# Kernel tuning notes

Hardware: AMD Instinct MI355X
Metric: run time of the kernel (lower is better)

Reference implementation:

```python
import jax, jax.numpy as jnp
import numpy as np

B, T, C = 4, 2048, 2048
N_HEAD = 16
HEAD_DIM = C // N_HEAD
ROPE_BASE = 10000.0


def setup_inputs() -> dict:
    key = jax.random.key(0)
    k1, k2, k3 = jax.random.split(key, 3)
    x = jax.random.normal(k1, (B, T, C), dtype=jnp.float32)
    Wqkv = jax.random.normal(k2, (C, 3 * C), dtype=jnp.float32) * 0.02
    bqkv = jnp.zeros((3 * C,), dtype=jnp.float32)
    Wproj = jax.random.normal(k3, (C, C), dtype=jnp.float32) * 0.02
    bproj = jnp.zeros((C,), dtype=jnp.float32)
    return {"x": x, "Wqkv": Wqkv, "bqkv": bqkv, "Wproj": Wproj, "bproj": bproj}


def _rope_cos_sin(seq_len, head_dim, dtype):
    inv_freq = 1.0 / (ROPE_BASE ** (jnp.arange(0, head_dim, 2, dtype=jnp.float32) / head_dim))
    t = jnp.arange(seq_len, dtype=jnp.float32)
    freqs = jnp.einsum("i,j->ij", t, inv_freq)          # [T, D/2]
    emb = jnp.concatenate([freqs, freqs], axis=-1)       # [T, D]
    return jnp.cos(emb).astype(dtype), jnp.sin(emb).astype(dtype)


def _rotate_half(x):
    half = x.shape[-1] // 2
    x1, x2 = x[..., :half], x[..., half:]
    return jnp.concatenate([-x2, x1], axis=-1)


def reference(x, Wqkv, bqkv, Wproj, bproj):
    b, t, c = x.shape
    qkv = x @ Wqkv + bqkv                                # [B, T, 3C]
    q, k, v = jnp.split(qkv, 3, axis=-1)
    # [B, T, C] -> [B, H, T, D]
    def to_heads(u):
        return u.reshape(b, t, N_HEAD, HEAD_DIM).transpose(0, 2, 1, 3)
    q, k, v = to_heads(q), to_heads(k), to_heads(v)
    cos, sin = _rope_cos_sin(t, HEAD_DIM, x.dtype)       # [T, D]
    cos = cos[None, None]                                # [1, 1, T, D]
    sin = sin[None, None]
    q = q * cos + _rotate_half(q) * sin
    k = k * cos + _rotate_half(k) * sin
    scale = 1.0 / np.sqrt(HEAD_DIM).astype(np.float32)
    scores = jnp.einsum("bhqd,bhkd->bhqk", q, k) * scale  # [B, H, T, T]
    causal = jnp.tril(jnp.ones((t, t), dtype=bool))
    scores = jnp.where(causal[None, None], scores, jnp.finfo(scores.dtype).min)
    att = jax.nn.softmax(scores, axis=-1)
    y = jnp.einsum("bhqk,bhkd->bhqd", att, v)             # [B, H, T, D]
    y = y.transpose(0, 2, 1, 3).reshape(b, t, c)
    return y @ Wproj + bproj
```

## Files before the change

kernel.cpp:

```cpp
#include <hip/hip_runtime.h>
#include <hip/hip_bf16.h>
#include <stdint.h>
#include <math.h>

#define NB 4
#define NT 2048
#define NC 2048
#define NH 16
#define HD 128
#define BT (NB*NT)

typedef __attribute__((ext_vector_type(8))) short s16x8;
typedef __attribute__((ext_vector_type(4))) short s16x4;
typedef __attribute__((ext_vector_type(4))) float f32x4;

typedef __attribute__((address_space(1))) void as1_void;
typedef __attribute__((address_space(3))) void as3_void;

static __device__ __forceinline__ unsigned short f2bf(float f) {
  union { float f; uint32_t u; } v; v.f = f;
  return (unsigned short)((v.u + 0x7fffu + ((v.u >> 16) & 1u)) >> 16);
}
static __device__ __forceinline__ float bf2f(unsigned short u) {
  union { uint32_t u; float f; } v; v.u = ((uint32_t)u) << 16;
  return v.f;
}
static __device__ __forceinline__ void async16(unsigned short* lds, const unsigned short* g) {
  __builtin_amdgcn_global_load_lds((as1_void*)g, (as3_void*)lds, 16, 0, 0);
}
static __device__ __forceinline__ uint32_t lds_off(void* p) {
  return (uint32_t)(size_t)(as3_void*)p;
}

__global__ void k_convert_bf16(const float* __restrict__ in, unsigned short* __restrict__ out, int n8) {
  int i = blockIdx.x * blockDim.x + threadIdx.x;
  if (i >= n8) return;
  const float4* p = (const float4*)in + (size_t)i * 2;
  float4 a = p[0], b = p[1];
  union { unsigned short s[8]; uint4 u; } o;
  o.s[0] = f2bf(a.x); o.s[1] = f2bf(a.y); o.s[2] = f2bf(a.z); o.s[3] = f2bf(a.w);
  o.s[4] = f2bf(b.x); o.s[5] = f2bf(b.y); o.s[6] = f2bf(b.z); o.s[7] = f2bf(b.w);
  ((uint4*)out)[i] = o.u;
}

__global__ void k_transpose_bf16(const float* __restrict__ W, unsigned short* __restrict__ WT, int K, int N) {
  __shared__ unsigned short tile[64][65];
  const int k0 = blockIdx.y * 64, n0 = blockIdx.x * 64;
  const int t = threadIdx.x;
  const int jj = t & 63, base_i = t >> 6;
  #pragma unroll
  for (int p = 0; p < 16; ++p) {
    int i = p * 4 + base_i;
    tile[i][jj] = f2bf(W[(size_t)(k0 + i) * N + n0 + jj]);
  }
  __syncthreads();
  #pragma unroll
  for (int p = 0; p < 16; ++p) {
    int j = p * 4 + base_i;
    WT[(size_t)(n0 + j) * K + k0 + jj] = tile[jj][j];
  }
}

__global__ void k_rope(unsigned short* __restrict__ Q, unsigned short* __restrict__ Kb) {
  int idx = blockIdx.x * 256 + threadIdx.x;
  int d = idx & 63;
  int tpos = (idx >> 6) & (NT - 1);
  int bh = idx >> 17;
  size_t o = ((size_t)bh * NT + tpos) * HD + d;
  float invf = exp2f(-(float)d * 0.2076205059304602f);
  float ang = (float)tpos * invf;
  float s, c;
  sincosf(ang, &s, &c);
  float q1 = bf2f(Q[o]),  q2 = bf2f(Q[o + 64]);
  float k1 = bf2f(Kb[o]), k2 = bf2f(Kb[o + 64]);
  const float qs = 0.08838834764831845f * 1.4426950408889634f;
  Q[o]       = f2bf((q1 * c - q2 * s) * qs);
  Q[o + 64]  = f2bf((q2 * c + q1 * s) * qs);
  Kb[o]      = f2bf(k1 * c - k2 * s);
  Kb[o + 64] = f2bf(k2 * c + k1 * s);
}

template<int MODE>
__global__ __launch_bounds__(256, 2)
void k_gemm_bt2(const unsigned short* __restrict__ A,
                const unsigned short* __restrict__ Bt,
                const float* __restrict__ bias,
                float* __restrict__ OutF,
                unsigned short* __restrict__ Qd,
                unsigned short* __restrict__ Kd,
                unsigned short* __restrict__ Vd,
                int M, int N, int K)
{
  __shared__ __align__(16) unsigned short Al[256 * 64];
  __shared__ __align__(16) unsigned short Bl[128 * 64];
  const int t = threadIdx.x;
  const int l = t & 63;
  const int wv = t >> 6;
  const int wm = wv >> 1, wn = wv & 1;
  const int bm = blockIdx.y * 256, bn = blockIdx.x * 128;
  const int lr = l & 15, lg = l >> 4;

  f32x4 acc[8][4];
  #pragma unroll
  for (int i = 0; i < 8; ++i)
    #pragma unroll
    for (int j = 0; j < 4; ++j)
      acc[i][j] = f32x4{0.f, 0.f, 0.f, 0.f};

  for (int k0 = 0; k0 < K; k0 += 64) {
    #pragma unroll
    for (int i = 0; i < 8; ++i) {
      const int Cc = i * 256 + t;
      const int row = Cc >> 3;
      const int kc = (Cc & 7) ^ (row & 7);
      async16(&Al[(i * 256 + (t & 192)) * 8], &A[(size_t)(bm + row) * K + k0 + kc * 8]);
    }
    #pragma unroll
    for (int i = 0; i < 4; ++i) {
      const int Cc = i * 256 + t;
      const int row = Cc >> 3;
      const int kc = (Cc & 7) ^ (row & 7);
      async16(&Bl[(i * 256 + (t & 192)) * 8], &Bt[(size_t)(bn + row) * K + k0 + kc * 8]);
    }
    __syncthreads();
    #pragma unroll
    for (int kk = 0; kk < 2; ++kk) {
      s16x8 af[8], bfr[4];
      #pragma unroll
      for (int mi = 0; mi < 8; ++mi) {
        const int row = wm * 128 + mi * 16 + lr;
        const int ch = (kk * 4 + lg) ^ (row & 7);
        af[mi] = *(const s16x8*)&Al[row * 64 + ch * 8];
      }
      #pragma unroll
      for (int ni = 0; ni < 4; ++ni) {
        const int row = wn * 64 + ni * 16 + lr;
        const int ch = (kk * 4 + lg) ^ (row & 7);
        bfr[ni] = *(const s16x8*)&Bl[row * 64 + ch * 8];
      }
      __builtin_amdgcn_s_setprio(1);
      #pragma unroll
      for (int mi = 0; mi < 8; ++mi)
        #pragma unroll
        for (int ni = 0; ni < 4; ++ni)
          acc[mi][ni] = __builtin_amdgcn_mfma_f32_16x16x32_bf16(af[mi], bfr[ni], acc[mi][ni], 0, 0, 0);
      __builtin_amdgcn_s_setprio(0);
    }
    __syncthreads();
  }

  #pragma unroll
  for (int mi = 0; mi < 8; ++mi) {
    #pragma unroll
    for (int ni = 0; ni < 4; ++ni) {
      const int col = bn + wn * 64 + ni * 16 + lr;
      const float bv = bias[col];
      #pragma unroll
      for (int r = 0; r < 4; ++r) {
        const int row = bm + wm * 128 + mi * 16 + lg * 4 + r;
        const float v = acc[mi][ni][r] + bv;
        if (MODE == 1) {
          OutF[(size_t)row * N + col] = v;
        } else {
          const int which = col >> 11;
          const int cc = col & 2047;
          const int h = cc >> 7, d = cc & 127;
          const int b = row >> 11, tp = row & 2047;
          unsigned short* dst = (which == 0) ? Qd : (which == 1 ? Kd : Vd);
          dst[(((size_t)(b * NH + h)) * NT + tp) * HD + d] = f2bf(v);
        }
      }
    }
  }
}

__global__ __launch_bounds__(256, 2)
void k_attn(const unsigned short* __restrict__ Q,
            const unsigned short* __restrict__ Kg,
            const unsigned short* __restrict__ Vg,
            unsigned short* __restrict__ Yatt)
{
  __shared__ __align__(16) unsigned short Kl[64 * 128];
  __shared__ __align__(16) unsigned short Vl[64 * 128];
  const int bh = blockIdx.x;
  const int pair = blockIdx.y;
  const int b = bh >> 4, h = bh & 15;
  const int t = threadIdx.x, l = t & 63, wv = t >> 6;
  const int lr = l & 15, lg = l >> 4;
  const size_t hoff = (size_t)bh * NT * HD;
  const unsigned short* Qh = Q + hoff;
  const unsigned short* Kh = Kg + hoff;
  const unsigned short* Vh = Vg + hoff;
  const uint32_t vbase = lds_off(Vl);

  #pragma unroll 1
  for (int rep = 0; rep < 2; ++rep) {
    const int qb = rep ? (31 - pair) : pair;
    const int q0w = qb * 64 + wv * 16;
    const int qrow = q0w + lr;

    s16x8 qf[4];
    #pragma unroll
    for (int m = 0; m < 4; ++m)
      qf[m] = *(const s16x8*)(Qh + (size_t)qrow * HD + m * 32 + lg * 8);

    f32x4 yt[8];
    #pragma unroll
    for (int n = 0; n < 8; ++n) yt[n] = f32x4{0.f, 0.f, 0.f, 0.f};
    float mrun = -1e30f, lrun = 0.f;

    const int nkv = qb + 1;
    for (int kv = 0; kv < nkv; ++kv) {
      const int kv0 = kv * 64;
      #pragma unroll
      for (int i = 0; i < 4; ++i) {
        const int Cc = i * 256 + t;
        {
          const int krow = Cc >> 4;
          const int kc = (Cc & 15) ^ (krow & 7);
          async16(&Kl[(i * 256 + (t & 192)) * 8], &Kh[(size_t)(kv0 + krow) * HD + kc * 8]);
        }
        {
          const int S = Cc >> 3, c8 = Cc & 7;
          const int kq = S >> 3, dq = S & 7;
          const int vk = kq * 4 + (c8 >> 1), vd = dq * 16 + (c8 & 1) * 8;
          async16(&Vl[(i * 256 + (t & 192)) * 8], &Vh[(size_t)(kv0 + vk) * HD + vd]);
        }
      }
      __syncthreads();

      f32x4 st[4];
      __builtin_amdgcn_s_setprio(1);
      #pragma unroll
      for (int kt = 0; kt < 4; ++kt) {
        f32x4 a = f32x4{0.f, 0.f, 0.f, 0.f};
        const int krow = kt * 16 + lr;
        #pragma unroll
        for (int m = 0; m < 4; ++m) {
          const int ch = (m * 4 + lg) ^ (krow & 7);
          s16x8 kf = *(const s16x8*)&Kl[krow * 128 + ch * 8];
          a = __builtin_amdgcn_mfma_f32_16x16x32_bf16(kf, qf[m], a, 0, 0, 0);
        }
        st[kt] = a;
      }
      __builtin_amdgcn_s_setprio(0);

      if (kv0 + 63 > q0w) {
        #pragma unroll
        for (int kt = 0; kt < 4; ++kt)
          #pragma unroll
          for (int r = 0; r < 4; ++r) {
            const int key = kv0 + kt * 16 + lg * 4 + r;
            if (key > qrow) st[kt][r] = -3.0e38f;
          }
      }

      float tm = -3.0e38f;
      #pragma unroll
      for (int kt = 0; kt < 4; ++kt)
        #pragma unroll
        for (int r = 0; r < 4; ++r) tm = fmaxf(tm, st[kt][r]);
      tm = fmaxf(tm, __shfl_xor(tm, 16));
      tm = fmaxf(tm, __shfl_xor(tm, 32));
      const float mnew = fmaxf(mrun, tm);
      const float fsc = exp2f(mrun - mnew);
      mrun = mnew;
      lrun *= fsc;
      #pragma unroll
      for (int n = 0; n < 8; ++n)
        #pragma unroll
        for (int r = 0; r < 4; ++r) yt[n][r] *= fsc;

      unsigned short pb[16];
      float psum = 0.f;
      #pragma unroll
      for (int kt = 0; kt < 4; ++kt)
        #pragma unroll
        for (int r = 0; r < 4; ++r) {
          const float p = exp2f(st[kt][r] - mnew);
          psum += p;
          pb[kt * 4 + r] = f2bf(p);
        }
      lrun += psum;

      s16x8 pf[2];
      #pragma unroll
      for (int gk = 0; gk < 2; ++gk)
        #pragma unroll
        for (int j = 0; j < 8; ++j)
          pf[gk][j] = (short)pb[(gk * 2 + (j >> 2)) * 4 + (j & 3)];

      #pragma unroll
      for (int gk = 0; gk < 2; ++gk) {
        s16x4 va[8], vb2[8];
        #pragma unroll
        for (int n = 0; n < 8; ++n) {
          const uint32_t a0 = vbase + ((uint32_t)((gk * 8 + lg) * 8 + n)) * 128 + (uint32_t)lr * 8;
          asm volatile("ds_read_b64_tr_b16 %0, %1" : "=v"(va[n])  : "v"(a0));
          asm volatile("ds_read_b64_tr_b16 %0, %1" : "=v"(vb2[n]) : "v"(a0 + 4096));
        }
        asm volatile("s_waitcnt lgkmcnt(0)" ::: "memory");
        __builtin_amdgcn_sched_barrier(0);
        __builtin_amdgcn_s_setprio(1);
        #pragma unroll
        for (int n = 0; n < 8; ++n) {
          s16x8 vf;
          vf[0] = va[n][0];  vf[1] = va[n][1];  vf[2] = va[n][2];  vf[3] = va[n][3];
          vf[4] = vb2[n][0]; vf[5] = vb2[n][1]; vf[6] = vb2[n][2]; vf[7] = vb2[n][3];
          yt[n] = __builtin_amdgcn_mfma_f32_16x16x32_bf16(vf, pf[gk], yt[n], 0, 0, 0);
        }
        __builtin_amdgcn_s_setprio(0);
      }
      __syncthreads();
    }

    lrun += __shfl_xor(lrun, 16);
    lrun += __shfl_xor(lrun, 32);
    const float inv = 1.f / lrun;
    unsigned short* yrow = Yatt + (size_t)(b * NT + q0w + lr) * NC + h * HD;
    #pragma unroll
    for (int n = 0; n < 8; ++n)
      #pragma unroll
      for (int r = 0; r < 4; ++r)
        yrow[n * 16 + lg * 4 + r] = f2bf(yt[n][r] * inv);
  }
}

extern "C" void kernel_launch(void* const* d_in, const int* in_sizes, int n_in,
                              void* d_out, int out_size, void* d_ws, size_t ws_size,
                              hipStream_t stream) {
  (void)in_sizes; (void)n_in; (void)out_size; (void)ws_size;
  const float* x     = (const float*)d_in[0];
  const float* Wqkv  = (const float*)d_in[1];
  const float* bqkv  = (const float*)d_in[2];
  const float* Wproj = (const float*)d_in[3];
  const float* bproj = (const float*)d_in[4];
  float* out = (float*)d_out;
  char* ws = (char*)d_ws;

  unsigned short* xb     = (unsigned short*)(ws);
  unsigned short* WqkvT  = (unsigned short*)(ws + 33554432);
  unsigned short* WprojT = (unsigned short*)(ws + 58720256);
  unsigned short* Qb     = (unsigned short*)(ws + 67108864);
  unsigned short* Kb     = (unsigned short*)(ws + 100663296);
  unsigned short* Vb     = (unsigned short*)(ws + 134217728);
  unsigned short* att    = xb;

  k_convert_bf16<<<dim3(8192), dim3(256), 0, stream>>>(x, xb, BT * NC / 8);
  k_transpose_bf16<<<dim3(96, 32), dim3(256), 0, stream>>>(Wqkv, WqkvT, NC, 3 * NC);
  k_transpose_bf16<<<dim3(32, 32), dim3(256), 0, stream>>>(Wproj, WprojT, NC, NC);
  k_gemm_bt2<0><<<dim3(48, 32), dim3(256), 0, stream>>>(xb, WqkvT, bqkv, nullptr, Qb, Kb, Vb, BT, 3 * NC, NC);
  k_rope<<<dim3(32768), dim3(256), 0, stream>>>(Qb, Kb);
  k_attn<<<dim3(64, 16), dim3(256), 0, stream>>>(Qb, Kb, Vb, att);
  k_gemm_bt2<1><<<dim3(16, 32), dim3(256), 0, stream>>>(att, WprojT, bproj, out, nullptr, nullptr, nullptr, BT, NC, NC);
}
```

Before: 446.6 us.

## Double-buffer K/V tiles in attention to overlap loads with compute

The attention kernel now keeps two LDS buffers for K and V and issues async loads for the next KV tile before computing the current one, with a single barrier per iteration. The goal is to hide global-to-LDS load latency behind the MFMA and softmax work. Two smaller changes ride along: the GEMM launch bound occupancy hint goes from 2 to 3 blocks, and the RoPE kernel uses the fast __sincosf intrinsic. The extra buffers double the attention kernel's LDS use, which can reduce occupancy. __sincosf is also less accurate for large angles.

Result: slower. 1.188 ms (+166.1%).

```diff
diff --git a/kernel.cpp b/kernel.cpp
--- a/kernel.cpp
+++ b/kernel.cpp
@@ -70,7 +70,7 @@
   float invf = exp2f(-(float)d * 0.2076205059304602f);
   float ang = (float)tpos * invf;
   float s, c;
-  sincosf(ang, &s, &c);
+  __sincosf(ang, &s, &c);
   float q1 = bf2f(Q[o]),  q2 = bf2f(Q[o + 64]);
   float k1 = bf2f(Kb[o]), k2 = bf2f(Kb[o + 64]);
   const float qs = 0.08838834764831845f * 1.4426950408889634f;
@@ -81,7 +81,7 @@
 }
 
 template<int MODE>
-__global__ __launch_bounds__(256, 2)
+__global__ __launch_bounds__(256, 3)
 void k_gemm_bt2(const unsigned short* __restrict__ A,
                 const unsigned short* __restrict__ Bt,
                 const float* __restrict__ bias,
@@ -180,8 +180,8 @@
             const unsigned short* __restrict__ Vg,
             unsigned short* __restrict__ Yatt)
 {
-  __shared__ __align__(16) unsigned short Kl[64 * 128];
-  __shared__ __align__(16) unsigned short Vl[64 * 128];
+  __shared__ __align__(16) unsigned short Kl[2][64 * 128];
+  __shared__ __align__(16) unsigned short Vl[2][64 * 128];
   const int bh = blockIdx.x;
   const int pair = blockIdx.y;
   const int b = bh >> 4, h = bh & 15;
@@ -191,7 +191,25 @@
   const unsigned short* Qh = Q + hoff;
   const unsigned short* Kh = Kg + hoff;
   const unsigned short* Vh = Vg + hoff;
-  const uint32_t vbase = lds_off(Vl);
+  const uint32_t vbase0 = lds_off(&Vl[0][0]);
+
+  auto stageKV = [&](int buf, int kv0) {
+    #pragma unroll
+    for (int i = 0; i < 4; ++i) {
+      const int Cc = i * 256 + t;
+      {
+        const int krow = Cc >> 4;
+        const int kc = (Cc & 15) ^ (krow & 7);
+        async16(&Kl[buf][(i * 256 + (t & 192)) * 8], &Kh[(size_t)(kv0 + krow) * HD + kc * 8]);
+      }
+      {
+        const int S = Cc >> 3, c8 = Cc & 7;
+        const int kq = S >> 3, dq = S & 7;
+        const int vk = kq * 4 + (c8 >> 1), vd = dq * 16 + (c8 & 1) * 8;
+        async16(&Vl[buf][(i * 256 + (t & 192)) * 8], &Vh[(size_t)(kv0 + vk) * HD + vd]);
+      }
+    }
+  };
 
   #pragma unroll 1
   for (int rep = 0; rep < 2; ++rep) {
@@ -199,6 +217,8 @@
     const int q0w = qb * 64 + wv * 16;
     const int qrow = q0w + lr;
 
+    __syncthreads();
+
     s16x8 qf[4];
     #pragma unroll
     for (int m = 0; m < 4; ++m)
@@ -209,26 +229,7 @@
     for (int n = 0; n < 8; ++n) yt[n] = f32x4{0.f, 0.f, 0.f, 0.f};
     float mrun = -1e30f, lrun = 0.f;
 
-    const int nkv = qb + 1;
-    for (int kv = 0; kv < nkv; ++kv) {
-      const int kv0 = kv * 64;
-      #pragma unroll
-      for (int i = 0; i < 4; ++i) {
-        const int Cc = i * 256 + t;
-        {
-          const int krow = Cc >> 4;
-          const int kc = (Cc & 15) ^ (krow & 7);
-          async16(&Kl[(i * 256 + (t & 192)) * 8], &Kh[(size_t)(kv0 + krow) * HD + kc * 8]);
-        }
-        {
-          const int S = Cc >> 3, c8 = Cc & 7;
-          const int kq = S >> 3, dq = S & 7;
-          const int vk = kq * 4 + (c8 >> 1), vd = dq * 16 + (c8 & 1) * 8;
-          async16(&Vl[(i * 256 + (t & 192)) * 8], &Vh[(size_t)(kv0 + vk) * HD + vd]);
-        }
-      }
-      __syncthreads();
-
+    auto computeTile = [&](int buf, int kv0) {
       f32x4 st[4];
       __builtin_amdgcn_s_setprio(1);
       #pragma unroll
@@ -238,7 +239,7 @@
         #pragma unroll
         for (int m = 0; m < 4; ++m) {
           const int ch = (m * 4 + lg) ^ (krow & 7);
-          s16x8 kf = *(const s16x8*)&Kl[krow * 128 + ch * 8];
+          s16x8 kf = *(const s16x8*)&Kl[buf][krow * 128 + ch * 8];
           a = __builtin_amdgcn_mfma_f32_16x16x32_bf16(kf, qf[m], a, 0, 0, 0);
         }
         st[kt] = a;
@@ -290,12 +291,13 @@
         for (int j = 0; j < 8; ++j)
           pf[gk][j] = (short)pb[(gk * 2 + (j >> 2)) * 4 + (j & 3)];
 
+      const uint32_t vb = vbase0 + (uint32_t)buf * 16384;
       #pragma unroll
       for (int gk = 0; gk < 2; ++gk) {
         s16x4 va[8], vb2[8];
         #pragma unroll
         for (int n = 0; n < 8; ++n) {
-          const uint32_t a0 = vbase + ((uint32_t)((gk * 8 + lg) * 8 + n)) * 128 + (uint32_t)lr * 8;
+          const uint32_t a0 = vb + ((uint32_t)((gk * 8 + lg) * 8 + n)) * 128 + (uint32_t)lr * 8;
           asm volatile("ds_read_b64_tr_b16 %0, %1" : "=v"(va[n])  : "v"(a0));
           asm volatile("ds_read_b64_tr_b16 %0, %1" : "=v"(vb2[n]) : "v"(a0 + 4096));
         }
@@ -311,8 +313,22 @@
         }
         __builtin_amdgcn_s_setprio(0);
       }
-      __syncthreads();
-    }
+    };
+
+    const int nkv = qb + 1;
+    stageKV(0, 0);
+    asm volatile("s_waitcnt vmcnt(0)" ::: "memory");
+    __syncthreads();
+    int buf = 0;
+    #pragma unroll 1
+    for (int kv = 0; kv < nkv - 1; ++kv) {
+      stageKV(buf ^ 1, (kv + 1) * 64);
+      computeTile(buf, kv * 64);
+      asm volatile("s_waitcnt vmcnt(0)" ::: "memory");
+      __builtin_amdgcn_s_barrier();
+      buf ^= 1;
+    }
+    computeTile(buf, (nkv - 1) * 64);
 
     lrun += __shfl_xor(lrun, 16);
     lrun += __shfl_xor(lrun, 32);
```
